# Kernel optimization log

Hardware: AMD Instinct MI355X
Metric: run time of the kernel (lower is better)

## Reference

```python
import jax, jax.numpy as jnp
import numpy as np

DILATIONS_REST = (2, 4, 8, 16, 32, 64)


def _causal_conv(x, v, g, b, dilation):
    # weight-norm: w = g * v / ||v||_(in,k) per out-channel
    norm = jnp.sqrt(jnp.sum(v * v, axis=(1, 2), keepdims=True))
    w = g[:, None, None] * v / norm                      # [O, I, K]
    pad = (v.shape[2] - 1) * dilation                    # left-only causal pad
    y = jax.lax.conv_general_dilated(
        x, w, window_strides=(1,), padding=[(pad, 0)],
        rhs_dilation=(dilation,), dimension_numbers=('NCH', 'OIH', 'NCH'))
    return y + b[None, :, None]


def setup_inputs() -> dict:
    key = jax.random.key(0)
    ks = jax.random.split(key, 16)
    B, T, V, E = 64, 2048, 32000, 300
    inp = {
        'inputs': jax.random.randint(ks[0], (B, T), 0, V),
        'de_feature': jax.random.normal(ks[1], (B, 11), dtype=jnp.float32),
        'emb': jax.random.normal(ks[2], (V, E), dtype=jnp.float32) * 0.02,
        'v0': jax.random.normal(ks[3], (128, 300, 5), dtype=jnp.float32) * 0.05,
        'g0': jnp.ones((128,), dtype=jnp.float32),
        'b0': jax.random.normal(ks[4], (128,), dtype=jnp.float32) * 0.01,
        'vr': jax.random.normal(ks[5], (6, 128, 128, 5), dtype=jnp.float32) * 0.05,
        'gr': jnp.ones((6, 128), dtype=jnp.float32),
        'br': jax.random.normal(ks[6], (6, 128), dtype=jnp.float32) * 0.01,
        'fc1_w': jax.random.normal(ks[7], (64, 139), dtype=jnp.float32) * 0.08,
        'fc1_b': jnp.zeros((64,), dtype=jnp.float32),
        'fc2_w': jax.random.normal(ks[8], (32, 64), dtype=jnp.float32) * 0.12,
        'fc2_b': jnp.zeros((32,), dtype=jnp.float32),
        'fc3_w': jax.random.normal(ks[9], (1, 32), dtype=jnp.float32) * 0.17,
        'fc3_b': jnp.zeros((1,), dtype=jnp.float32),
    }
    return inp


def reference(inputs, de_feature, emb, v0, g0, b0, vr, gr, br,
              fc1_w, fc1_b, fc2_w, fc2_b, fc3_w, fc3_b):
    x = emb[inputs]                       # [B, T, 300]
    x = jnp.transpose(x, (0, 2, 1))       # [B, 300, T]
    x = jax.nn.relu(_causal_conv(x, v0, g0, b0, 1))
    for i, d in enumerate(DILATIONS_REST):
        x = jax.nn.relu(_causal_conv(x, vr[i], gr[i], br[i], d))
    emb_v = x[:, :, -1]                   # last timestep [B, 128]
    combo = jnp.concatenate([emb_v, de_feature], axis=1)  # [B, 139]
    h = jax.nn.relu(combo @ fc1_w.T + fc1_b)
    h = jax.nn.relu(h @ fc2_w.T + fc2_b)
    logits = h @ fc3_w.T + fc3_b          # [B, 1]
    return logits
```

## Files before the change

kernel.cpp:

```cpp
#include <hip/hip_runtime.h>


typedef __attribute__((ext_vector_type(8))) short bfrag8;
typedef __attribute__((ext_vector_type(4))) float floatx4;
typedef __attribute__((ext_vector_type(4))) short short4v;
typedef __attribute__((ext_vector_type(4))) float float4v;

__device__ __forceinline__ unsigned short f2bf(float f) {
  union { float f; unsigned u; } v; v.f = f;
  unsigned r = v.u + 0x7fffu + ((v.u >> 16) & 1u);
  return (unsigned short)(r >> 16);
}
__device__ __forceinline__ float bf2f(unsigned short h) {
  union { unsigned u; float f; } v; v.u = ((unsigned)h) << 16;
  return v.f;
}
__device__ __forceinline__ int swz(int row) { return ((row >> 1) & 7) << 4; }

__global__ __launch_bounds__(512)
void k_wnorm(const float* __restrict__ v0, const float* __restrict__ g0,
             const float* __restrict__ vr, const float* __restrict__ gr,
             unsigned short* __restrict__ WB0, unsigned short* __restrict__ WBr) {
  const int gw = (blockIdx.x << 3) + (threadIdx.x >> 6);
  const int lane = threadIdx.x & 63;
  if (gw < 128) {
    const int o = gw;
    const float* v = v0 + o * 1500;
    float ss = 0.f;
    for (int i = lane; i < 1500; i += 64) { const float x = v[i]; ss += x * x; }
#pragma unroll
    for (int off = 32; off; off >>= 1) ss += __shfl_xor(ss, off, 64);
    const float scale = g0[o] * rsqrtf(ss);
    const int ot = o >> 4;
    for (int kk = lane; kk < 1600; kk += 64) {
      const int tap = kk / 320, c = kk % 320;
      const float w = (c < 300) ? v[c * 5 + tap] * scale : 0.f;
      const int ks = kk >> 5;
      const int li = (o & 15) | (((kk >> 3) & 3) << 4);
      WB0[(((ot * 50 + ks) * 64 + li) << 3) | (kk & 7)] = f2bf(w);
    }
  } else {
    const int idx = gw - 128;
    const int l = idx >> 7, o = idx & 127;
    const float* v = vr + (size_t)(l * 128 + o) * 640;
    float ss = 0.f;
#pragma unroll
    for (int i = 0; i < 10; ++i) { const float x = v[lane + (i << 6)]; ss += x * x; }
#pragma unroll
    for (int off = 32; off; off >>= 1) ss += __shfl_xor(ss, off, 64);
    const float scale = gr[l * 128 + o] * rsqrtf(ss);
    unsigned short* WB = WBr + (size_t)l * 81920;
    const int ot = o >> 4;
#pragma unroll
    for (int i = 0; i < 10; ++i) {
      const int kk = lane + (i << 6);
      const int tap = kk >> 7, c = kk & 127;
      const float w = v[c * 5 + tap] * scale;
      const int ks = kk >> 5;
      const int li = (o & 15) | (((kk >> 3) & 3) << 4);
      WB[(((ot * 20 + ks) * 64 + li) << 3) | (kk & 7)] = f2bf(w);
    }
  }
}

__global__ __launch_bounds__(512, 4)
void k_conv0g(const int* __restrict__ tokens, const float* __restrict__ emb,
              const unsigned short* __restrict__ WB0, const float* __restrict__ b0,
              unsigned short* __restrict__ A0) {
  __shared__ char embBuf[67 * 656];
  __shared__ int toks[68];
  const int tid = threadIdx.x;
  const int qt = blockIdx.x, b = blockIdx.y;
  if (tid < 68) {
    const int p = (qt << 6) + tid;
    toks[tid] = (tid < 67 && p < 509) ? tokens[(b << 11) + 1539 + p] : -1;
  }
  __syncthreads();
  for (int idx = tid; idx < 67 * 80; idx += 512) {
    const int r = idx / 80, s = idx - r * 80;
    short4v o = {0, 0, 0, 0};
    const int tok = toks[r];
    if (tok >= 0 && s < 75) {
      const float4v v = *(const float4v*)(emb + (size_t)tok * 300 + (s << 2));
      o[0] = (short)f2bf(v[0]); o[1] = (short)f2bf(v[1]);
      o[2] = (short)f2bf(v[2]); o[3] = (short)f2bf(v[3]);
    }
    *(short4v*)(embBuf + r * 656 + (s << 3)) = o;
  }
  __syncthreads();
  const int lane = tid & 63, w = tid >> 6;
  const int qb = lane & 15, kg = lane >> 4;
  floatx4 acc[2];
  acc[0] = floatx4{0.f, 0.f, 0.f, 0.f};
  acc[1] = floatx4{0.f, 0.f, 0.f, 0.f};
  const unsigned short* wb0 = WB0 + (size_t)(((w * 50) << 6) + lane) * 8;
#pragma unroll
  for (int tap = 0; tap < 5; ++tap) {
    bfrag8 bf[10];
#pragma unroll
    for (int cs = 0; cs < 10; ++cs)
      bf[cs] = *(const bfrag8*)(wb0 + ((tap * 10 + cs) << 9));
#pragma unroll
    for (int cs = 0; cs < 10; ++cs) {
      const int cb = (cs << 6) + (kg << 4);
#pragma unroll
      for (int m = 0; m < 2; ++m) {
        const int row = (((m << 4) + qb) << 1) + tap;
        const bfrag8 a = *(const bfrag8*)(embBuf + row * 656 + cb);
        acc[m] = __builtin_amdgcn_mfma_f32_16x16x32_bf16(a, bf[cs], acc[m], 0, 0, 0);
      }
    }
  }
  unsigned short* ob = A0 + (((size_t)b << 8) + (qt << 5)) * 128;
  const int o = (w << 4) + qb;
  const float bv = b0[o];
#pragma unroll
  for (int m = 0; m < 2; ++m)
#pragma unroll
    for (int r = 0; r < 4; ++r) {
      const int ql = (m << 4) + (kg << 2) + r;
      ob[ql * 128 + o] = f2bf(fmaxf(acc[m][r] + bv, 0.f));
    }
}

template<int NMTW, int NOTW, int MCAP>
__device__ __forceinline__ void conv_l(const char* bi, char* bo,
    const unsigned short* __restrict__ WBl, const float* __restrict__ bias,
    int mt0, int og, int qb, int kg, int lane) {
  floatx4 acc[NMTW][NOTW];
#pragma unroll
  for (int m = 0; m < NMTW; ++m)
#pragma unroll
    for (int j = 0; j < NOTW; ++j) acc[m][j] = floatx4{0.f, 0.f, 0.f, 0.f};
#pragma unroll
  for (int tap = 0; tap < 5; ++tap) {
    bfrag8 bfs[NOTW][4];
#pragma unroll
    for (int j = 0; j < NOTW; ++j)
#pragma unroll
      for (int cs = 0; cs < 4; ++cs)
        bfs[j][cs] = *(const bfrag8*)(WBl +
            (size_t)((((og * NOTW + j) * 20 + (tap << 2) + cs) << 6) + lane) * 8);
#pragma unroll
    for (int cs = 0; cs < 4; ++cs) {
      const int cb = (cs << 6) + (kg << 4);
#pragma unroll
      for (int m = 0; m < NMTW; ++m) {
        const int row = (((mt0 + m) << 4) + qb) * 2 + tap;
        const bfrag8 a = *(const bfrag8*)(bi + (((row << 8) + cb) ^ swz(row)));
#pragma unroll
        for (int j = 0; j < NOTW; ++j)
          acc[m][j] = __builtin_amdgcn_mfma_f32_16x16x32_bf16(a, bfs[j][cs], acc[m][j], 0, 0, 0);
      }
    }
  }
#pragma unroll
  for (int m = 0; m < NMTW; ++m)
#pragma unroll
    for (int j = 0; j < NOTW; ++j) {
      const int o = ((og * NOTW + j) << 4) + qb;
      const float bv = bias[o];
#pragma unroll
      for (int r = 0; r < 4; ++r) {
        const int qq = ((mt0 + m) << 4) + (kg << 2) + r;
        if (qq < MCAP)
          *(unsigned short*)(bo + (((qq << 8) + (o << 1)) ^ swz(qq))) =
              f2bf(fmaxf(acc[m][j][r] + bv, 0.f));
      }
    }
}

__global__ __launch_bounds__(512, 1)
void k_conv12(const unsigned short* __restrict__ A0,
              const unsigned short* __restrict__ WBr, const float* __restrict__ br,
              unsigned short* __restrict__ L2out) {
  __shared__ char a0stage[100 * 256];
  __shared__ char l1buf[36 * 256];
  const int tid = threadIdx.x;
  const int qt = blockIdx.x, b = blockIdx.y;
  const char* a0b = (const char*)(A0 + ((size_t)b << 15));
  for (int idx = tid; idx < 100 * 16; idx += 512) {
    const int r = idx >> 4, s = idx & 15;
    float4v v = {0.f, 0.f, 0.f, 0.f};
    if (r < 73) {
      int rs = (qt << 6) + r; if (rs > 255) rs = 255;
      v = *(const float4v*)(a0b + (rs << 8) + (s << 4));
    }
    *(float4v*)(a0stage + (((r << 8) + (s << 4)) ^ swz(r))) = v;
  }
  __syncthreads();
  const int lane = tid & 63, w = tid >> 6;
  const int og = w & 3, mgh = w >> 2;
  const int qb = lane & 15, kg = lane >> 4;
  if (mgh == 0) conv_l<2, 2, 36>(a0stage, l1buf, WBr, br, 0, og, qb, kg, lane);
  else          conv_l<1, 2, 36>(a0stage, l1buf, WBr, br, 2, og, qb, kg, lane);
  __syncthreads();
  {
    floatx4 acc = {0.f, 0.f, 0.f, 0.f};
    const unsigned short* wbl = WBr + 81920;
#pragma unroll
    for (int tap = 0; tap < 5; ++tap) {
      bfrag8 bfs[4];
#pragma unroll
      for (int cs = 0; cs < 4; ++cs)
        bfs[cs] = *(const bfrag8*)(wbl +
            (size_t)(((w * 20 + (tap << 2) + cs) << 6) + lane) * 8);
#pragma unroll
      for (int cs = 0; cs < 4; ++cs) {
        const int cb = (cs << 6) + (kg << 4);
        const int row = (qb << 1) + tap;
        const bfrag8 a = *(const bfrag8*)(l1buf + (((row << 8) + cb) ^ swz(row)));
        acc = __builtin_amdgcn_mfma_f32_16x16x32_bf16(a, bfs[cs], acc, 0, 0, 0);
      }
    }
    const int o = (w << 4) + qb;
    const float bv = br[128 + o];
    unsigned short* ob = L2out + ((size_t)b << 13);
#pragma unroll
    for (int r = 0; r < 4; ++r) {
      const int q2 = (qt << 4) + (kg << 2) + r;
      if (q2 < 61) ob[(q2 << 7) + o] = f2bf(fmaxf(acc[r] + bv, 0.f));
    }
  }
}

__global__ __launch_bounds__(512, 1)
void k_tail3(const unsigned short* __restrict__ L2out, const unsigned short* __restrict__ WBr,
             const float* __restrict__ br, const float* __restrict__ de,
             const float* __restrict__ w1, const float* __restrict__ b1,
             const float* __restrict__ w2, const float* __restrict__ b2,
             const float* __restrict__ w3, const float* __restrict__ b3,
             float* __restrict__ out) {
  __shared__ char lds2[68 * 256 + 36 * 256 + 384];
  char* bufS = lds2;
  char* bufT = lds2 + 68 * 256;
  float* h1 = (float*)(lds2 + 68 * 256 + 36 * 256);
  float* h2 = h1 + 64;
  const int tid = threadIdx.x, b = blockIdx.x;
  const int lane = tid & 63, w = tid >> 6;
  const int qb = lane & 15, kg = lane >> 4;

  const char* l2b = (const char*)(L2out + ((size_t)b << 13));
  for (int idx = tid; idx < 61 * 16; idx += 512) {
    const int r = idx >> 4, s = idx & 15;
    *(float4v*)(bufS + (((r << 8) + (s << 4)) ^ swz(r))) =
        *(const float4v*)(l2b + (r << 8) + (s << 4));
  }
  __syncthreads();

  conv_l<1, 2, 32>(bufS, bufT, WBr + 2 * 81920, br + 256, w & 1, w >> 1, qb, kg, lane);
  __syncthreads();
  conv_l<1, 1, 16>(bufT, bufS, WBr + 3 * 81920, br + 384, 0, w, qb, kg, lane);
  __syncthreads();
  conv_l<1, 1, 16>(bufS, bufT, WBr + 4 * 81920, br + 512, 0, w, qb, kg, lane);
  __syncthreads();
  conv_l<1, 1, 16>(bufT, bufS, WBr + 5 * 81920, br + 640, 0, w, qb, kg, lane);
  __syncthreads();

  const unsigned short* o6 = (const unsigned short*)bufS;
  {
    const int o1 = tid >> 3, part = tid & 7;
    const int j0 = part * 18;
    const int j1 = (j0 + 18 < 139) ? j0 + 18 : 139;
    float s = 0.f;
    const float* wrow = w1 + o1 * 139;
    for (int j = j0; j < j1; ++j) {
      const float x = (j < 128) ? bf2f(o6[j]) : de[b * 11 + (j - 128)];
      s += wrow[j] * x;
    }
    s += __shfl_down(s, 4, 64);
    s += __shfl_down(s, 2, 64);
    s += __shfl_down(s, 1, 64);
    if (part == 0) h1[o1] = fmaxf(s + b1[o1], 0.f);
  }
  __syncthreads();
  if (tid < 64) {
    const int o2 = tid >> 1, part = tid & 1;
    float s = 0.f;
    const float* wrow = w2 + o2 * 64 + part * 32;
    for (int j = 0; j < 32; ++j) s += wrow[j] * h1[part * 32 + j];
    s += __shfl_down(s, 1, 64);
    if (part == 0) h2[o2] = fmaxf(s + b2[o2], 0.f);
  }
  __syncthreads();
  if (tid < 32) {
    float s = w3[tid] * h2[tid];
    s += __shfl_down(s, 16, 64);
    s += __shfl_down(s, 8, 64);
    s += __shfl_down(s, 4, 64);
    s += __shfl_down(s, 2, 64);
    s += __shfl_down(s, 1, 64);
    if (tid == 0) out[b] = s + b3[0];
  }
}

extern "C" void kernel_launch(void* const* d_in, const int* in_sizes, int n_in,
                              void* d_out, int out_size, void* d_ws, size_t ws_size,
                              hipStream_t stream) {
  const int*   tokens = (const int*)  d_in[0];
  const float* de     = (const float*)d_in[1];
  const float* emb    = (const float*)d_in[2];
  const float* v0     = (const float*)d_in[3];
  const float* g0     = (const float*)d_in[4];
  const float* b0     = (const float*)d_in[5];
  const float* vr     = (const float*)d_in[6];
  const float* gr     = (const float*)d_in[7];
  const float* br     = (const float*)d_in[8];
  const float* w1     = (const float*)d_in[9];
  const float* b1     = (const float*)d_in[10];
  const float* w2     = (const float*)d_in[11];
  const float* b2     = (const float*)d_in[12];
  const float* w3     = (const float*)d_in[13];
  const float* b3     = (const float*)d_in[14];
  float* out = (float*)d_out;

  char* w = (char*)d_ws;
  unsigned short* WB0   = (unsigned short*)(w + 0);
  unsigned short* WBr   = (unsigned short*)(w + 409600);
  unsigned short* A0    = (unsigned short*)(w + 1392640);
  unsigned short* L2out = (unsigned short*)(w + 5586944);

  hipLaunchKernelGGL(k_wnorm, dim3(112), dim3(512), 0, stream, v0, g0, vr, gr, WB0, WBr);
  hipLaunchKernelGGL(k_conv0g, dim3(8, 64), dim3(512), 0, stream,
                     tokens, emb, WB0, b0, A0);
  hipLaunchKernelGGL(k_conv12, dim3(4, 64), dim3(512), 0, stream, A0, WBr, br, L2out);
  hipLaunchKernelGGL(k_tail3, dim3(64), dim3(512), 0, stream,
                     L2out, WBr, br, de, w1, b1, w2, b2, w3, b3, out);
}
```

Baseline: 65.83 us.

## Fuse all four kernels into one cooperative kernel with grid syncs

Replaces the four separate launches (weight norm, conv0, conv1-2, tail) with a single cooperative kernel of 256 blocks that uses grid.sync between phases. Conv0 is re-tiled so each block handles 64 output positions instead of 32, matching the 256-block grid. The goal is to remove launch overhead and inter-kernel gaps. In exchange, the tail phase runs on only 64 of 256 blocks, conv0 runs with fewer and larger blocks at occupancy 1, and grid-wide barriers add their own cost.

```diff
diff --git a/kernel.cpp b/kernel.cpp
--- a/kernel.cpp
+++ b/kernel.cpp
@@ -1,4 +1,7 @@
 #include <hip/hip_runtime.h>
+#include <hip/hip_cooperative_groups.h>
+
+namespace cg = cooperative_groups;
 
 
 typedef __attribute__((ext_vector_type(8))) short bfrag8;
@@ -16,112 +19,6 @@
   return v.f;
 }
 __device__ __forceinline__ int swz(int row) { return ((row >> 1) & 7) << 4; }
-
-__global__ __launch_bounds__(512)
-void k_wnorm(const float* __restrict__ v0, const float* __restrict__ g0,
-             const float* __restrict__ vr, const float* __restrict__ gr,
-             unsigned short* __restrict__ WB0, unsigned short* __restrict__ WBr) {
-  const int gw = (blockIdx.x << 3) + (threadIdx.x >> 6);
-  const int lane = threadIdx.x & 63;
-  if (gw < 128) {
-    const int o = gw;
-    const float* v = v0 + o * 1500;
-    float ss = 0.f;
-    for (int i = lane; i < 1500; i += 64) { const float x = v[i]; ss += x * x; }
-#pragma unroll
-    for (int off = 32; off; off >>= 1) ss += __shfl_xor(ss, off, 64);
-    const float scale = g0[o] * rsqrtf(ss);
-    const int ot = o >> 4;
-    for (int kk = lane; kk < 1600; kk += 64) {
-      const int tap = kk / 320, c = kk % 320;
-      const float w = (c < 300) ? v[c * 5 + tap] * scale : 0.f;
-      const int ks = kk >> 5;
-      const int li = (o & 15) | (((kk >> 3) & 3) << 4);
-      WB0[(((ot * 50 + ks) * 64 + li) << 3) | (kk & 7)] = f2bf(w);
-    }
-  } else {
-    const int idx = gw - 128;
-    const int l = idx >> 7, o = idx & 127;
-    const float* v = vr + (size_t)(l * 128 + o) * 640;
-    float ss = 0.f;
-#pragma unroll
-    for (int i = 0; i < 10; ++i) { const float x = v[lane + (i << 6)]; ss += x * x; }
-#pragma unroll
-    for (int off = 32; off; off >>= 1) ss += __shfl_xor(ss, off, 64);
-    const float scale = gr[l * 128 + o] * rsqrtf(ss);
-    unsigned short* WB = WBr + (size_t)l * 81920;
-    const int ot = o >> 4;
-#pragma unroll
-    for (int i = 0; i < 10; ++i) {
-      const int kk = lane + (i << 6);
-      const int tap = kk >> 7, c = kk & 127;
-      const float w = v[c * 5 + tap] * scale;
-      const int ks = kk >> 5;
-      const int li = (o & 15) | (((kk >> 3) & 3) << 4);
-      WB[(((ot * 20 + ks) * 64 + li) << 3) | (kk & 7)] = f2bf(w);
-    }
-  }
-}
-
-__global__ __launch_bounds__(512, 4)
-void k_conv0g(const int* __restrict__ tokens, const float* __restrict__ emb,
-              const unsigned short* __restrict__ WB0, const float* __restrict__ b0,
-              unsigned short* __restrict__ A0) {
-  __shared__ char embBuf[67 * 656];
-  __shared__ int toks[68];
-  const int tid = threadIdx.x;
-  const int qt = blockIdx.x, b = blockIdx.y;
-  if (tid < 68) {
-    const int p = (qt << 6) + tid;
-    toks[tid] = (tid < 67 && p < 509) ? tokens[(b << 11) + 1539 + p] : -1;
-  }
-  __syncthreads();
-  for (int idx = tid; idx < 67 * 80; idx += 512) {
-    const int r = idx / 80, s = idx - r * 80;
-    short4v o = {0, 0, 0, 0};
-    const int tok = toks[r];
-    if (tok >= 0 && s < 75) {
-      const float4v v = *(const float4v*)(emb + (size_t)tok * 300 + (s << 2));
-      o[0] = (short)f2bf(v[0]); o[1] = (short)f2bf(v[1]);
-      o[2] = (short)f2bf(v[2]); o[3] = (short)f2bf(v[3]);
-    }
-    *(short4v*)(embBuf + r * 656 + (s << 3)) = o;
-  }
-  __syncthreads();
-  const int lane = tid & 63, w = tid >> 6;
-  const int qb = lane & 15, kg = lane >> 4;
-  floatx4 acc[2];
-  acc[0] = floatx4{0.f, 0.f, 0.f, 0.f};
-  acc[1] = floatx4{0.f, 0.f, 0.f, 0.f};
-  const unsigned short* wb0 = WB0 + (size_t)(((w * 50) << 6) + lane) * 8;
-#pragma unroll
-  for (int tap = 0; tap < 5; ++tap) {
-    bfrag8 bf[10];
-#pragma unroll
-    for (int cs = 0; cs < 10; ++cs)
-      bf[cs] = *(const bfrag8*)(wb0 + ((tap * 10 + cs) << 9));
-#pragma unroll
-    for (int cs = 0; cs < 10; ++cs) {
-      const int cb = (cs << 6) + (kg << 4);
-#pragma unroll
-      for (int m = 0; m < 2; ++m) {
-        const int row = (((m << 4) + qb) << 1) + tap;
-        const bfrag8 a = *(const bfrag8*)(embBuf + row * 656 + cb);
-        acc[m] = __builtin_amdgcn_mfma_f32_16x16x32_bf16(a, bf[cs], acc[m], 0, 0, 0);
-      }
-    }
-  }
-  unsigned short* ob = A0 + (((size_t)b << 8) + (qt << 5)) * 128;
-  const int o = (w << 4) + qb;
-  const float bv = b0[o];
-#pragma unroll
-  for (int m = 0; m < 2; ++m)
-#pragma unroll
-    for (int r = 0; r < 4; ++r) {
-      const int ql = (m << 4) + (kg << 2) + r;
-      ob[ql * 128 + o] = f2bf(fmaxf(acc[m][r] + bv, 0.f));
-    }
-}
 
 template<int NMTW, int NOTW, int MCAP>
 __device__ __forceinline__ void conv_l(const char* bi, char* bo,
@@ -171,31 +68,140 @@
 }
 
 __global__ __launch_bounds__(512, 1)
-void k_conv12(const unsigned short* __restrict__ A0,
-              const unsigned short* __restrict__ WBr, const float* __restrict__ br,
-              unsigned short* __restrict__ L2out) {
-  __shared__ char a0stage[100 * 256];
-  __shared__ char l1buf[36 * 256];
+void k_all(const int* __restrict__ tokens, const float* __restrict__ emb,
+           const float* __restrict__ v0, const float* __restrict__ g0,
+           const float* __restrict__ vr, const float* __restrict__ gr,
+           const float* __restrict__ b0, const float* __restrict__ br,
+           const float* __restrict__ de,
+           const float* __restrict__ w1, const float* __restrict__ b1,
+           const float* __restrict__ w2, const float* __restrict__ b2,
+           const float* __restrict__ w3, const float* __restrict__ b3,
+           unsigned short* __restrict__ WB0, unsigned short* __restrict__ WBr,
+           unsigned short* __restrict__ A0, unsigned short* __restrict__ L2out,
+           float* __restrict__ out) {
+  __shared__ char lds[87808];
+  cg::grid_group grid = cg::this_grid();
   const int tid = threadIdx.x;
-  const int qt = blockIdx.x, b = blockIdx.y;
-  const char* a0b = (const char*)(A0 + ((size_t)b << 15));
-  for (int idx = tid; idx < 100 * 16; idx += 512) {
-    const int r = idx >> 4, s = idx & 15;
-    float4v v = {0.f, 0.f, 0.f, 0.f};
-    if (r < 73) {
-      int rs = (qt << 6) + r; if (rs > 255) rs = 255;
-      v = *(const float4v*)(a0b + (rs << 8) + (s << 4));
-    }
-    *(float4v*)(a0stage + (((r << 8) + (s << 4)) ^ swz(r))) = v;
-  }
-  __syncthreads();
+  const int bx = blockIdx.x;
+  const int qt = bx & 3, b = bx >> 2;
   const int lane = tid & 63, w = tid >> 6;
-  const int og = w & 3, mgh = w >> 2;
   const int qb = lane & 15, kg = lane >> 4;
-  if (mgh == 0) conv_l<2, 2, 36>(a0stage, l1buf, WBr, br, 0, og, qb, kg, lane);
-  else          conv_l<1, 2, 36>(a0stage, l1buf, WBr, br, 2, og, qb, kg, lane);
-  __syncthreads();
+
   {
+    const int gw = (bx << 3) + w;
+    if (gw < 128) {
+      const int o = gw;
+      const float* v = v0 + o * 1500;
+      float ss = 0.f;
+      for (int i = lane; i < 1500; i += 64) { const float x = v[i]; ss += x * x; }
+#pragma unroll
+      for (int off = 32; off; off >>= 1) ss += __shfl_xor(ss, off, 64);
+      const float scale = g0[o] * rsqrtf(ss);
+      const int ot = o >> 4;
+      for (int kk = lane; kk < 1600; kk += 64) {
+        const int tap = kk / 320, c = kk % 320;
+        const float wv = (c < 300) ? v[c * 5 + tap] * scale : 0.f;
+        const int ks = kk >> 5;
+        const int li = (o & 15) | (((kk >> 3) & 3) << 4);
+        WB0[(((ot * 50 + ks) * 64 + li) << 3) | (kk & 7)] = f2bf(wv);
+      }
+    } else if (gw < 896) {
+      const int idx = gw - 128;
+      const int l = idx >> 7, o = idx & 127;
+      const float* v = vr + (size_t)(l * 128 + o) * 640;
+      float ss = 0.f;
+#pragma unroll
+      for (int i = 0; i < 10; ++i) { const float x = v[lane + (i << 6)]; ss += x * x; }
+#pragma unroll
+      for (int off = 32; off; off >>= 1) ss += __shfl_xor(ss, off, 64);
+      const float scale = gr[l * 128 + o] * rsqrtf(ss);
+      unsigned short* WB = WBr + (size_t)l * 81920;
+      const int ot = o >> 4;
+#pragma unroll
+      for (int i = 0; i < 10; ++i) {
+        const int kk = lane + (i << 6);
+        const int tap = kk >> 7, c = kk & 127;
+        const float wv = v[c * 5 + tap] * scale;
+        const int ks = kk >> 5;
+        const int li = (o & 15) | (((kk >> 3) & 3) << 4);
+        WB[(((ot * 20 + ks) * 64 + li) << 3) | (kk & 7)] = f2bf(wv);
+      }
+    }
+  }
+  grid.sync();
+
+  {
+    char* embBuf = lds;
+    int* toks = (int*)(lds + 87248);
+    if (tid < 134) {
+      const int p = (qt << 7) + tid;
+      toks[tid] = (tid < 133 && p < 509) ? tokens[(b << 11) + 1539 + p] : -1;
+    }
+    __syncthreads();
+    for (int idx = tid; idx < 133 * 80; idx += 512) {
+      const int r = idx / 80, s = idx - r * 80;
+      short4v o = {0, 0, 0, 0};
+      const int tok = toks[r];
+      if (tok >= 0 && s < 75) {
+        const float4v v = *(const float4v*)(emb + (size_t)tok * 300 + (s << 2));
+        o[0] = (short)f2bf(v[0]); o[1] = (short)f2bf(v[1]);
+        o[2] = (short)f2bf(v[2]); o[3] = (short)f2bf(v[3]);
+      }
+      *(short4v*)(embBuf + r * 656 + (s << 3)) = o;
+    }
+    __syncthreads();
+    floatx4 acc[4];
+#pragma unroll
+    for (int m = 0; m < 4; ++m) acc[m] = floatx4{0.f, 0.f, 0.f, 0.f};
+    const unsigned short* wb0 = WB0 + (size_t)(((w * 50) << 6) + lane) * 8;
+#pragma unroll
+    for (int tap = 0; tap < 5; ++tap) {
+      bfrag8 bf[10];
+#pragma unroll
+      for (int cs = 0; cs < 10; ++cs)
+        bf[cs] = *(const bfrag8*)(wb0 + ((tap * 10 + cs) << 9));
+#pragma unroll
+      for (int cs = 0; cs < 10; ++cs) {
+        const int cb = (cs << 6) + (kg << 4);
+#pragma unroll
+        for (int m = 0; m < 4; ++m) {
+          const int row = (((m << 4) + qb) << 1) + tap;
+          const bfrag8 a = *(const bfrag8*)(embBuf + row * 656 + cb);
+          acc[m] = __builtin_amdgcn_mfma_f32_16x16x32_bf16(a, bf[cs], acc[m], 0, 0, 0);
+        }
+      }
+    }
+    unsigned short* ob = A0 + (((size_t)b << 8) + (qt << 6)) * 128;
+    const int o = (w << 4) + qb;
+    const float bv = b0[o];
+#pragma unroll
+    for (int m = 0; m < 4; ++m)
+#pragma unroll
+      for (int r = 0; r < 4; ++r) {
+        const int ql = (m << 4) + (kg << 2) + r;
+        ob[ql * 128 + o] = f2bf(fmaxf(acc[m][r] + bv, 0.f));
+      }
+  }
+  grid.sync();
+
+  {
+    char* a0stage = lds;
+    char* l1buf = lds + 25600;
+    const char* a0b = (const char*)(A0 + ((size_t)b << 15));
+    for (int idx = tid; idx < 100 * 16; idx += 512) {
+      const int r = idx >> 4, s = idx & 15;
+      float4v v = {0.f, 0.f, 0.f, 0.f};
+      if (r < 73) {
+        int rs = (qt << 6) + r; if (rs > 255) rs = 255;
+        v = *(const float4v*)(a0b + (rs << 8) + (s << 4));
+      }
+      *(float4v*)(a0stage + (((r << 8) + (s << 4)) ^ swz(r))) = v;
+    }
+    __syncthreads();
+    const int og = w & 3, mgh = w >> 2;
+    if (mgh == 0) conv_l<2, 2, 36>(a0stage, l1buf, WBr, br, 0, og, qb, kg, lane);
+    else          conv_l<1, 2, 36>(a0stage, l1buf, WBr, br, 2, og, qb, kg, lane);
+    __syncthreads();
     floatx4 acc = {0.f, 0.f, 0.f, 0.f};
     const unsigned short* wbl = WBr + 81920;
 #pragma unroll
@@ -222,75 +228,65 @@
       if (q2 < 61) ob[(q2 << 7) + o] = f2bf(fmaxf(acc[r] + bv, 0.f));
     }
   }
-}
-
-__global__ __launch_bounds__(512, 1)
-void k_tail3(const unsigned short* __restrict__ L2out, const unsigned short* __restrict__ WBr,
-             const float* __restrict__ br, const float* __restrict__ de,
-             const float* __restrict__ w1, const float* __restrict__ b1,
-             const float* __restrict__ w2, const float* __restrict__ b2,
-             const float* __restrict__ w3, const float* __restrict__ b3,
-             float* __restrict__ out) {
-  __shared__ char lds2[68 * 256 + 36 * 256 + 384];
-  char* bufS = lds2;
-  char* bufT = lds2 + 68 * 256;
-  float* h1 = (float*)(lds2 + 68 * 256 + 36 * 256);
-  float* h2 = h1 + 64;
-  const int tid = threadIdx.x, b = blockIdx.x;
-  const int lane = tid & 63, w = tid >> 6;
-  const int qb = lane & 15, kg = lane >> 4;
-
-  const char* l2b = (const char*)(L2out + ((size_t)b << 13));
-  for (int idx = tid; idx < 61 * 16; idx += 512) {
-    const int r = idx >> 4, s = idx & 15;
-    *(float4v*)(bufS + (((r << 8) + (s << 4)) ^ swz(r))) =
-        *(const float4v*)(l2b + (r << 8) + (s << 4));
-  }
-  __syncthreads();
-
-  conv_l<1, 2, 32>(bufS, bufT, WBr + 2 * 81920, br + 256, w & 1, w >> 1, qb, kg, lane);
-  __syncthreads();
-  conv_l<1, 1, 16>(bufT, bufS, WBr + 3 * 81920, br + 384, 0, w, qb, kg, lane);
-  __syncthreads();
-  conv_l<1, 1, 16>(bufS, bufT, WBr + 4 * 81920, br + 512, 0, w, qb, kg, lane);
-  __syncthreads();
-  conv_l<1, 1, 16>(bufT, bufS, WBr + 5 * 81920, br + 640, 0, w, qb, kg, lane);
-  __syncthreads();
-
-  const unsigned short* o6 = (const unsigned short*)bufS;
-  {
-    const int o1 = tid >> 3, part = tid & 7;
-    const int j0 = part * 18;
-    const int j1 = (j0 + 18 < 139) ? j0 + 18 : 139;
-    float s = 0.f;
-    const float* wrow = w1 + o1 * 139;
-    for (int j = j0; j < j1; ++j) {
-      const float x = (j < 128) ? bf2f(o6[j]) : de[b * 11 + (j - 128)];
-      s += wrow[j] * x;
-    }
-    s += __shfl_down(s, 4, 64);
-    s += __shfl_down(s, 2, 64);
-    s += __shfl_down(s, 1, 64);
-    if (part == 0) h1[o1] = fmaxf(s + b1[o1], 0.f);
-  }
-  __syncthreads();
-  if (tid < 64) {
-    const int o2 = tid >> 1, part = tid & 1;
-    float s = 0.f;
-    const float* wrow = w2 + o2 * 64 + part * 32;
-    for (int j = 0; j < 32; ++j) s += wrow[j] * h1[part * 32 + j];
-    s += __shfl_down(s, 1, 64);
-    if (part == 0) h2[o2] = fmaxf(s + b2[o2], 0.f);
-  }
-  __syncthreads();
-  if (tid < 32) {
-    float s = w3[tid] * h2[tid];
-    s += __shfl_down(s, 16, 64);
-    s += __shfl_down(s, 8, 64);
-    s += __shfl_down(s, 4, 64);
-    s += __shfl_down(s, 2, 64);
-    s += __shfl_down(s, 1, 64);
-    if (tid == 0) out[b] = s + b3[0];
+  grid.sync();
+
+  if (qt == 0) {
+    char* bufS = lds;
+    char* bufT = lds + 17408;
+    float* h1 = (float*)(lds + 26624);
+    float* h2 = h1 + 64;
+    const char* l2b = (const char*)(L2out + ((size_t)b << 13));
+    for (int idx = tid; idx < 61 * 16; idx += 512) {
+      const int r = idx >> 4, s = idx & 15;
+      *(float4v*)(bufS + (((r << 8) + (s << 4)) ^ swz(r))) =
+          *(const float4v*)(l2b + (r << 8) + (s << 4));
+    }
+    __syncthreads();
+
+    conv_l<1, 2, 32>(bufS, bufT, WBr + 2 * 81920, br + 256, w & 1, w >> 1, qb, kg, lane);
+    __syncthreads();
+    conv_l<1, 1, 16>(bufT, bufS, WBr + 3 * 81920, br + 384, 0, w, qb, kg, lane);
+    __syncthreads();
+    conv_l<1, 1, 16>(bufS, bufT, WBr + 4 * 81920, br + 512, 0, w, qb, kg, lane);
+    __syncthreads();
+    conv_l<1, 1, 16>(bufT, bufS, WBr + 5 * 81920, br + 640, 0, w, qb, kg, lane);
+    __syncthreads();
+
+    const unsigned short* o6 = (const unsigned short*)bufS;
+    {
+      const int o1 = tid >> 3, part = tid & 7;
+      const int j0 = part * 18;
+      const int j1 = (j0 + 18 < 139) ? j0 + 18 : 139;
+      float s = 0.f;
+      const float* wrow = w1 + o1 * 139;
+      for (int j = j0; j < j1; ++j) {
+        const float x = (j < 128) ? bf2f(o6[j]) : de[b * 11 + (j - 128)];
+        s += wrow[j] * x;
+      }
+      s += __shfl_down(s, 4, 64);
+      s += __shfl_down(s, 2, 64);
+      s += __shfl_down(s, 1, 64);
+      if (part == 0) h1[o1] = fmaxf(s + b1[o1], 0.f);
+    }
+    __syncthreads();
+    if (tid < 64) {
+      const int o2 = tid >> 1, part = tid & 1;
+      float s = 0.f;
+      const float* wrow = w2 + o2 * 64 + part * 32;
+      for (int j = 0; j < 32; ++j) s += wrow[j] * h1[part * 32 + j];
+      s += __shfl_down(s, 1, 64);
+      if (part == 0) h2[o2] = fmaxf(s + b2[o2], 0.f);
+    }
+    __syncthreads();
+    if (tid < 32) {
+      float s = w3[tid] * h2[tid];
+      s += __shfl_down(s, 16, 64);
+      s += __shfl_down(s, 8, 64);
+      s += __shfl_down(s, 4, 64);
+      s += __shfl_down(s, 2, 64);
+      s += __shfl_down(s, 1, 64);
+      if (tid == 0) out[b] = s + b3[0];
+    }
   }
 }
 
@@ -312,18 +308,21 @@
   const float* b2     = (const float*)d_in[12];
   const float* w3     = (const float*)d_in[13];
   const float* b3     = (const float*)d_in[14];
-  float* out = (float*)d_out;
-
-  char* w = (char*)d_ws;
-  unsigned short* WB0   = (unsigned short*)(w + 0);
-  unsigned short* WBr   = (unsigned short*)(w + 409600);
-  unsigned short* A0    = (unsigned short*)(w + 1392640);
-  unsigned short* L2out = (unsigned short*)(w + 5586944);
-
-  hipLaunchKernelGGL(k_wnorm, dim3(112), dim3(512), 0, stream, v0, g0, vr, gr, WB0, WBr);
-  hipLaunchKernelGGL(k_conv0g, dim3(8, 64), dim3(512), 0, stream,
-                     tokens, emb, WB0, b0, A0);
-  hipLaunchKernelGGL(k_conv12, dim3(4, 64), dim3(512), 0, stream, A0, WBr, br, L2out);
-  hipLaunchKernelGGL(k_tail3, dim3(64), dim3(512), 0, stream,
-                     L2out, WBr, br, de, w1, b1, w2, b2, w3, b3, out);
-}
+  float* outp = (float*)d_out;
+
+  char* ws = (char*)d_ws;
+  unsigned short* WB0   = (unsigned short*)(ws + 0);
+  unsigned short* WBr   = (unsigned short*)(ws + 409600);
+  unsigned short* A0    = (unsigned short*)(ws + 1392640);
+  unsigned short* L2out = (unsigned short*)(ws + 5586944);
+
+  void* args[] = {
+    (void*)&tokens, (void*)&emb,
+    (void*)&v0, (void*)&g0, (void*)&vr, (void*)&gr,
+    (void*)&b0, (void*)&br, (void*)&de,
+    (void*)&w1, (void*)&b1, (void*)&w2, (void*)&b2, (void*)&w3, (void*)&b3,
+    (void*)&WB0, (void*)&WBr, (void*)&A0, (void*)&L2out, (void*)&outp
+  };
+  hipLaunchCooperativeKernel((const void*)k_all, dim3(256), dim3(512),
+                             args, 0, stream);
+}
```

Result: slower. 158.0 us (+140.0%).

## Fuse conv layers 1-6 and MLP head into one per-batch kernel

Applied to the files above, without the earlier changes.

Merges the separate conv1/conv2 kernel and the tail kernel into a single kernel with one block per batch element. The block stages all 253 receptive-field rows of A0 in LDS and runs all six dilated conv layers plus the MLP in place, with no L2out round trip and one fewer launch. It also restructures the embedding gather in conv0 so each thread handles contiguous 40-float chunks of a row, replacing the per-element divide. The cost is that the first two layers now run on only 64 blocks instead of 256, and each block uses about 118KB of LDS, which lowers parallelism.

```diff
diff --git a/kernel.cpp b/kernel.cpp
--- a/kernel.cpp
+++ b/kernel.cpp
@@ -76,16 +76,32 @@
     toks[tid] = (tid < 67 && p < 509) ? tokens[(b << 11) + 1539 + p] : -1;
   }
   __syncthreads();
-  for (int idx = tid; idx < 67 * 80; idx += 512) {
-    const int r = idx / 80, s = idx - r * 80;
-    short4v o = {0, 0, 0, 0};
-    const int tok = toks[r];
-    if (tok >= 0 && s < 75) {
-      const float4v v = *(const float4v*)(emb + (size_t)tok * 300 + (s << 2));
-      o[0] = (short)f2bf(v[0]); o[1] = (short)f2bf(v[1]);
-      o[2] = (short)f2bf(v[2]); o[3] = (short)f2bf(v[3]);
-    }
-    *(short4v*)(embBuf + r * 656 + (s << 3)) = o;
+#pragma unroll
+  for (int pass = 0; pass < 2; ++pass) {
+    const int r = (pass << 6) + (tid >> 3);
+    if (r < 67) {
+      const int e = tid & 7;
+      const int tok = toks[r];
+      char* dst = embBuf + r * 656 + e * 80;
+      if (tok >= 0) {
+        const float* src = emb + (size_t)tok * 300 + e * 40;
+#pragma unroll
+        for (int k = 0; k < 10; ++k) {
+          const int s = e * 10 + k;
+          short4v o = {0, 0, 0, 0};
+          if (s < 75) {
+            const float4v v = *(const float4v*)(src + (k << 2));
+            o[0] = (short)f2bf(v[0]); o[1] = (short)f2bf(v[1]);
+            o[2] = (short)f2bf(v[2]); o[3] = (short)f2bf(v[3]);
+          }
+          *(short4v*)(dst + (k << 3)) = o;
+        }
+      } else {
+#pragma unroll
+        for (int k = 0; k < 10; ++k)
+          *(short4v*)(dst + (k << 3)) = short4v{0, 0, 0, 0};
+      }
+    }
   }
   __syncthreads();
   const int lane = tid & 63, w = tid >> 6;
@@ -171,93 +187,44 @@
 }
 
 __global__ __launch_bounds__(512, 1)
-void k_conv12(const unsigned short* __restrict__ A0,
-              const unsigned short* __restrict__ WBr, const float* __restrict__ br,
-              unsigned short* __restrict__ L2out) {
-  __shared__ char a0stage[100 * 256];
-  __shared__ char l1buf[36 * 256];
-  const int tid = threadIdx.x;
-  const int qt = blockIdx.x, b = blockIdx.y;
-  const char* a0b = (const char*)(A0 + ((size_t)b << 15));
-  for (int idx = tid; idx < 100 * 16; idx += 512) {
-    const int r = idx >> 4, s = idx & 15;
-    float4v v = {0.f, 0.f, 0.f, 0.f};
-    if (r < 73) {
-      int rs = (qt << 6) + r; if (rs > 255) rs = 255;
-      v = *(const float4v*)(a0b + (rs << 8) + (s << 4));
-    }
-    *(float4v*)(a0stage + (((r << 8) + (s << 4)) ^ swz(r))) = v;
-  }
-  __syncthreads();
-  const int lane = tid & 63, w = tid >> 6;
-  const int og = w & 3, mgh = w >> 2;
-  const int qb = lane & 15, kg = lane >> 4;
-  if (mgh == 0) conv_l<2, 2, 36>(a0stage, l1buf, WBr, br, 0, og, qb, kg, lane);
-  else          conv_l<1, 2, 36>(a0stage, l1buf, WBr, br, 2, og, qb, kg, lane);
-  __syncthreads();
-  {
-    floatx4 acc = {0.f, 0.f, 0.f, 0.f};
-    const unsigned short* wbl = WBr + 81920;
-#pragma unroll
-    for (int tap = 0; tap < 5; ++tap) {
-      bfrag8 bfs[4];
-#pragma unroll
-      for (int cs = 0; cs < 4; ++cs)
-        bfs[cs] = *(const bfrag8*)(wbl +
-            (size_t)(((w * 20 + (tap << 2) + cs) << 6) + lane) * 8);
-#pragma unroll
-      for (int cs = 0; cs < 4; ++cs) {
-        const int cb = (cs << 6) + (kg << 4);
-        const int row = (qb << 1) + tap;
-        const bfrag8 a = *(const bfrag8*)(l1buf + (((row << 8) + cb) ^ swz(row)));
-        acc = __builtin_amdgcn_mfma_f32_16x16x32_bf16(a, bfs[cs], acc, 0, 0, 0);
-      }
-    }
-    const int o = (w << 4) + qb;
-    const float bv = br[128 + o];
-    unsigned short* ob = L2out + ((size_t)b << 13);
-#pragma unroll
-    for (int r = 0; r < 4; ++r) {
-      const int q2 = (qt << 4) + (kg << 2) + r;
-      if (q2 < 61) ob[(q2 << 7) + o] = f2bf(fmaxf(acc[r] + bv, 0.f));
-    }
-  }
-}
-
-__global__ __launch_bounds__(512, 1)
-void k_tail3(const unsigned short* __restrict__ L2out, const unsigned short* __restrict__ WBr,
-             const float* __restrict__ br, const float* __restrict__ de,
-             const float* __restrict__ w1, const float* __restrict__ b1,
-             const float* __restrict__ w2, const float* __restrict__ b2,
-             const float* __restrict__ w3, const float* __restrict__ b3,
-             float* __restrict__ out) {
-  __shared__ char lds2[68 * 256 + 36 * 256 + 384];
-  char* bufS = lds2;
-  char* bufT = lds2 + 68 * 256;
-  float* h1 = (float*)(lds2 + 68 * 256 + 36 * 256);
+void k_rest512(const unsigned short* __restrict__ A0, const unsigned short* __restrict__ WBr,
+               const float* __restrict__ br, const float* __restrict__ de,
+               const float* __restrict__ w1, const float* __restrict__ b1,
+               const float* __restrict__ w2, const float* __restrict__ b2,
+               const float* __restrict__ w3, const float* __restrict__ b3,
+               float* __restrict__ out) {
+  __shared__ char lds[66560 + 33536 + 17408 + 384];
+  char* bufIn = lds;
+  char* actP  = lds + 66560;
+  char* actQ  = lds + 100096;
+  float* h1 = (float*)(lds + 117504);
   float* h2 = h1 + 64;
   const int tid = threadIdx.x, b = blockIdx.x;
   const int lane = tid & 63, w = tid >> 6;
   const int qb = lane & 15, kg = lane >> 4;
 
-  const char* l2b = (const char*)(L2out + ((size_t)b << 13));
-  for (int idx = tid; idx < 61 * 16; idx += 512) {
+  const char* a0b = (const char*)(A0 + ((size_t)b << 15));
+  for (int idx = tid; idx < 253 * 16; idx += 512) {
     const int r = idx >> 4, s = idx & 15;
-    *(float4v*)(bufS + (((r << 8) + (s << 4)) ^ swz(r))) =
-        *(const float4v*)(l2b + (r << 8) + (s << 4));
-  }
-  __syncthreads();
-
-  conv_l<1, 2, 32>(bufS, bufT, WBr + 2 * 81920, br + 256, w & 1, w >> 1, qb, kg, lane);
-  __syncthreads();
-  conv_l<1, 1, 16>(bufT, bufS, WBr + 3 * 81920, br + 384, 0, w, qb, kg, lane);
-  __syncthreads();
-  conv_l<1, 1, 16>(bufS, bufT, WBr + 4 * 81920, br + 512, 0, w, qb, kg, lane);
-  __syncthreads();
-  conv_l<1, 1, 16>(bufT, bufS, WBr + 5 * 81920, br + 640, 0, w, qb, kg, lane);
-  __syncthreads();
-
-  const unsigned short* o6 = (const unsigned short*)bufS;
+    *(float4v*)(bufIn + (((r << 8) + (s << 4)) ^ swz(r))) =
+        *(const float4v*)(a0b + (r << 8) + (s << 4));
+  }
+  __syncthreads();
+
+  conv_l<2, 4, 128>(bufIn, actP, WBr + 0 * 81920, br + 0,   (w & 3) * 2, w >> 2, qb, kg, lane);
+  __syncthreads();
+  conv_l<1, 4, 64>(actP, actQ, WBr + 1 * 81920, br + 128, w & 3, w >> 2, qb, kg, lane);
+  __syncthreads();
+  conv_l<1, 2, 32>(actQ, actP, WBr + 2 * 81920, br + 256, w & 1, w >> 1, qb, kg, lane);
+  __syncthreads();
+  conv_l<1, 1, 16>(actP, actQ, WBr + 3 * 81920, br + 384, 0, w, qb, kg, lane);
+  __syncthreads();
+  conv_l<1, 1, 16>(actQ, actP, WBr + 4 * 81920, br + 512, 0, w, qb, kg, lane);
+  __syncthreads();
+  conv_l<1, 1, 16>(actP, actQ, WBr + 5 * 81920, br + 640, 0, w, qb, kg, lane);
+  __syncthreads();
+
+  const unsigned short* o6 = (const unsigned short*)actQ;
   {
     const int o1 = tid >> 3, part = tid & 7;
     const int j0 = part * 18;
@@ -315,15 +282,13 @@
   float* out = (float*)d_out;
 
   char* w = (char*)d_ws;
-  unsigned short* WB0   = (unsigned short*)(w + 0);
-  unsigned short* WBr   = (unsigned short*)(w + 409600);
-  unsigned short* A0    = (unsigned short*)(w + 1392640);
-  unsigned short* L2out = (unsigned short*)(w + 5586944);
+  unsigned short* WB0 = (unsigned short*)(w + 0);
+  unsigned short* WBr = (unsigned short*)(w + 409600);
+  unsigned short* A0  = (unsigned short*)(w + 1392640);
 
   hipLaunchKernelGGL(k_wnorm, dim3(112), dim3(512), 0, stream, v0, g0, vr, gr, WB0, WBr);
   hipLaunchKernelGGL(k_conv0g, dim3(8, 64), dim3(512), 0, stream,
                      tokens, emb, WB0, b0, A0);
-  hipLaunchKernelGGL(k_conv12, dim3(4, 64), dim3(512), 0, stream, A0, WBr, br, L2out);
-  hipLaunchKernelGGL(k_tail3, dim3(64), dim3(512), 0, stream,
-                     L2out, WBr, br, de, w1, b1, w2, b2, w3, b3, out);
-}
+  hipLaunchKernelGGL(k_rest512, dim3(64), dim3(512), 0, stream,
+                     A0, WBr, br, de, w1, b1, w2, b2, w3, b3, out);
+}
```

New measurement: 70.94 us. +7.8%, slower.

## Fuse tail layers into conv12 via last-block-per-batch atomic counter

Applied to the files above, without the earlier changes.

Merges the k_tail3 kernel into k_conv12 using a per-batch atomic counter. The last of the four q-tile blocks for each batch runs the remaining conv layers and the MLP head. Counters are zeroed in k_wnorm. This removes one kernel launch and the gap between launches, and lets the tail overlap with other batches' conv12 work. The cost is threadfences, an atomic per block, and tail work serialized on one block per batch.

```diff
diff --git a/kernel.cpp b/kernel.cpp
--- a/kernel.cpp
+++ b/kernel.cpp
@@ -20,7 +20,9 @@
 __global__ __launch_bounds__(512)
 void k_wnorm(const float* __restrict__ v0, const float* __restrict__ g0,
              const float* __restrict__ vr, const float* __restrict__ gr,
-             unsigned short* __restrict__ WB0, unsigned short* __restrict__ WBr) {
+             unsigned short* __restrict__ WB0, unsigned short* __restrict__ WBr,
+             int* __restrict__ counters) {
+  if (blockIdx.x == 0 && threadIdx.x < 64) counters[threadIdx.x] = 0;
   const int gw = (blockIdx.x << 3) + (threadIdx.x >> 6);
   const int lane = threadIdx.x & 63;
   if (gw < 128) {
@@ -171,11 +173,18 @@
 }
 
 __global__ __launch_bounds__(512, 1)
-void k_conv12(const unsigned short* __restrict__ A0,
-              const unsigned short* __restrict__ WBr, const float* __restrict__ br,
-              unsigned short* __restrict__ L2out) {
-  __shared__ char a0stage[100 * 256];
-  __shared__ char l1buf[36 * 256];
+void k_conv12f(const unsigned short* __restrict__ A0,
+               const unsigned short* __restrict__ WBr, const float* __restrict__ br,
+               unsigned short* __restrict__ L2out, int* __restrict__ counters,
+               const float* __restrict__ de,
+               const float* __restrict__ w1, const float* __restrict__ b1,
+               const float* __restrict__ w2, const float* __restrict__ b2,
+               const float* __restrict__ w3, const float* __restrict__ b3,
+               float* __restrict__ out) {
+  __shared__ char arena[34816];
+  __shared__ int isLast;
+  char* a0stage = arena;
+  char* l1buf   = arena + 25600;
   const int tid = threadIdx.x;
   const int qt = blockIdx.x, b = blockIdx.y;
   const char* a0b = (const char*)(A0 + ((size_t)b << 15));
@@ -222,24 +231,16 @@
       if (q2 < 61) ob[(q2 << 7) + o] = f2bf(fmaxf(acc[r] + bv, 0.f));
     }
   }
-}
-
-__global__ __launch_bounds__(512, 1)
-void k_tail3(const unsigned short* __restrict__ L2out, const unsigned short* __restrict__ WBr,
-             const float* __restrict__ br, const float* __restrict__ de,
-             const float* __restrict__ w1, const float* __restrict__ b1,
-             const float* __restrict__ w2, const float* __restrict__ b2,
-             const float* __restrict__ w3, const float* __restrict__ b3,
-             float* __restrict__ out) {
-  __shared__ char lds2[68 * 256 + 36 * 256 + 384];
-  char* bufS = lds2;
-  char* bufT = lds2 + 68 * 256;
-  float* h1 = (float*)(lds2 + 68 * 256 + 36 * 256);
+  __threadfence();
+  if (tid == 0) isLast = (atomicAdd(&counters[b], 1) == 3);
+  __syncthreads();
+  if (!isLast) return;
+  __threadfence();
+
+  char* bufS = arena;
+  char* bufT = arena + 17408;
+  float* h1 = (float*)(arena + 26624);
   float* h2 = h1 + 64;
-  const int tid = threadIdx.x, b = blockIdx.x;
-  const int lane = tid & 63, w = tid >> 6;
-  const int qb = lane & 15, kg = lane >> 4;
-
   const char* l2b = (const char*)(L2out + ((size_t)b << 13));
   for (int idx = tid; idx < 61 * 16; idx += 512) {
     const int r = idx >> 4, s = idx & 15;
@@ -319,11 +320,13 @@
   unsigned short* WBr   = (unsigned short*)(w + 409600);
   unsigned short* A0    = (unsigned short*)(w + 1392640);
   unsigned short* L2out = (unsigned short*)(w + 5586944);
-
-  hipLaunchKernelGGL(k_wnorm, dim3(112), dim3(512), 0, stream, v0, g0, vr, gr, WB0, WBr);
+  int* counters         = (int*)(w + 6635520);
+
+  hipLaunchKernelGGL(k_wnorm, dim3(112), dim3(512), 0, stream,
+                     v0, g0, vr, gr, WB0, WBr, counters);
   hipLaunchKernelGGL(k_conv0g, dim3(8, 64), dim3(512), 0, stream,
                      tokens, emb, WB0, b0, A0);
-  hipLaunchKernelGGL(k_conv12, dim3(4, 64), dim3(512), 0, stream, A0, WBr, br, L2out);
-  hipLaunchKernelGGL(k_tail3, dim3(64), dim3(512), 0, stream,
-                     L2out, WBr, br, de, w1, b1, w2, b2, w3, b3, out);
-}
+  hipLaunchKernelGGL(k_conv12f, dim3(4, 64), dim3(512), 0, stream,
+                     A0, WBr, br, L2out, counters,
+                     de, w1, b1, w2, b2, w3, b3, out);
+}
```

After: 114.1 us. 73.3% more time.
